# Kernel tuning notes

Measured on AMD Instinct MI355X. Metric: run time of the kernel, lower is better.

Reference implementation:

```python
import jax, jax.numpy as jnp
import numpy as np

N_HEADS = 16
KV_HEADS = 4
HEAD_DIM = 128
D_MODEL = N_HEADS * HEAD_DIM  # 2048
KV_DIM = KV_HEADS * HEAD_DIM  # 512
MAX_POS = 4096
ROPE_THETA = 10000.0
EPS = 1e-5


def _rope_cache(seq_len):
    # QEffMolmoRotaryEmbedding: inv_freq over head_dim, emb = cat(freqs, freqs)
    inv_freq = 1.0 / (ROPE_THETA ** (jnp.arange(0, HEAD_DIM, 2, dtype=jnp.float32) / HEAD_DIM))
    t = jnp.arange(seq_len, dtype=jnp.float32)
    freqs = jnp.outer(t, inv_freq)                      # [S, D/2]
    emb = jnp.concatenate([freqs, freqs], axis=-1)      # [S, D]
    return jnp.cos(emb), jnp.sin(emb)


def _rotate_half(x):
    # x: [B, H, T, D] -> cat(-x2, x1) with halves along last dim
    x1, x2 = jnp.split(x, 2, axis=-1)
    return jnp.concatenate([-x2, x1], axis=-1)


def _rms_norm(x, w):
    var = jnp.mean(jnp.square(x), axis=-1, keepdims=True)
    return (x * jax.lax.rsqrt(var + EPS)) * w


def setup_inputs() -> dict:
    key = jax.random.key(0)
    ks = jax.random.split(key, 8)
    B, T = 1, 2048
    q = jax.random.normal(ks[0], (B, T, D_MODEL), dtype=jnp.float32)
    k = jax.random.normal(ks[1], (B, T, KV_DIM), dtype=jnp.float32)
    v = jax.random.normal(ks[2], (B, T, KV_DIM), dtype=jnp.float32)
    # causal mask: True means masked (torch.where(mask, -10000, scores))
    attention_mask = jnp.triu(jnp.ones((T, T), dtype=bool), k=1)[None, None]  # [1,1,T,T]
    position_ids = jnp.arange(T, dtype=jnp.int32)[None, :]                    # [B,T]
    q_norm_w = jax.random.normal(ks[3], (D_MODEL,), dtype=jnp.float32) * 0.02 + 1.0
    k_norm_w = jax.random.normal(ks[4], (KV_DIM,), dtype=jnp.float32) * 0.02 + 1.0
    w_out = jax.random.normal(ks[5], (D_MODEL, D_MODEL), dtype=jnp.float32) * (D_MODEL ** -0.5)
    return {"q": q, "k": k, "v": v, "attention_mask": attention_mask,
            "position_ids": position_ids, "q_norm_w": q_norm_w,
            "k_norm_w": k_norm_w, "w_out": w_out}


def reference(q, k, v, attention_mask, position_ids, q_norm_w, k_norm_w, w_out):
    B, T, C = q.shape
    # QK-norm on flat projections
    q = _rms_norm(q, q_norm_w)
    k = _rms_norm(k, k_norm_w)
    # split heads: [B, H, T, D]
    q = q.reshape(B, T, N_HEADS, HEAD_DIM).transpose(0, 2, 1, 3)
    k = k.reshape(B, T, KV_HEADS, HEAD_DIM).transpose(0, 2, 1, 3)
    v = v.reshape(B, T, KV_HEADS, HEAD_DIM).transpose(0, 2, 1, 3)
    # RoPE (rotate_half variant)
    cos_c, sin_c = _rope_cache(MAX_POS)
    cos = cos_c[position_ids][:, None]  # [B,1,T,D]
    sin = sin_c[position_ids][:, None]
    q = q * cos + _rotate_half(q) * sin
    k = k * cos + _rotate_half(k) * sin
    # GQA expand
    rep = N_HEADS // KV_HEADS
    k = jnp.repeat(k, rep, axis=1)
    v = jnp.repeat(v, rep, axis=1)
    scale = 1.0 / np.sqrt(HEAD_DIM)
    scores = jnp.einsum('bhqd,bhkd->bhqk', q, k) * scale  # [B,H,T,T]
    scores = jnp.where(attention_mask, jnp.float32(-10000.0), scores)
    attn = jax.nn.softmax(scores.astype(jnp.float32), axis=-1).astype(q.dtype)
    out = jnp.einsum('bhqk,bhkd->bhqd', attn, v)          # [B,H,T,D]
    out = out.transpose(0, 2, 1, 3).reshape(B, T, C)
    return out @ w_out.T
```

## Files before the change

kernel.cpp:

```cpp
#include <hip/hip_runtime.h>
#include <hip/hip_bf16.h>
#include <math.h>

#define T_SEQ 2048
#define NH 16
#define KVH 4
#define HD 128
#define DM 2048
#define KVD 512

typedef short bf16x8 __attribute__((ext_vector_type(8)));
typedef float f32x4 __attribute__((ext_vector_type(4)));
typedef float f32x16 __attribute__((ext_vector_type(16)));
typedef unsigned int uint2v __attribute__((ext_vector_type(2)));

static __device__ __forceinline__ unsigned short f2bf(float f) {
    unsigned int x = __float_as_uint(f);
    x += 0x7fff + ((x >> 16) & 1);
    return (unsigned short)(x >> 16);
}
static __device__ __forceinline__ float bf2f(unsigned short u) {
    return __uint_as_float(((unsigned int)u) << 16);
}

static __device__ __forceinline__ unsigned int cvtpk(float lo, float hi) {
    unsigned int r;
    asm("v_cvt_pk_bf16_f32 %0, %1, %2" : "=v"(r) : "v"(lo), "v"(hi));
    return r;
}

static __device__ __forceinline__ f32x4 mfma16(bf16x8 a, bf16x8 b, f32x4 c) {
    return __builtin_amdgcn_mfma_f32_16x16x32_bf16(a, b, c, 0, 0, 0);
}
static __device__ __forceinline__ f32x16 mfma32(bf16x8 a, bf16x8 b, f32x16 c) {
    return __builtin_amdgcn_mfma_f32_32x32x16_bf16(a, b, c, 0, 0, 0);
}

static __device__ __forceinline__ void gl_lds16(const unsigned short* g, unsigned short* l) {
    __builtin_amdgcn_global_load_lds(
        (const __attribute__((address_space(1))) unsigned int*)g,
        (__attribute__((address_space(3))) unsigned int*)l,
        16, 0, 0);
}


__global__ __launch_bounds__(256) void qk_prep(
    const float* __restrict__ q, const float* __restrict__ k,
    const float* __restrict__ qw, const float* __restrict__ kw,
    const int* __restrict__ pos_ids,
    unsigned short* __restrict__ Qb, unsigned short* __restrict__ Ks) {
    __shared__ float qr[DM];
    __shared__ float kr[KVD];
    __shared__ float cosL[64], sinL[64];
    __shared__ float redq[4], redk[4];
    int t = blockIdx.x, tid = threadIdx.x;

    float qs = 0.f, ks = 0.f;
    {
        const float* qp = q + (size_t)t * DM + tid * 8;
        float4 v0 = *(const float4*)(qp);
        float4 v1 = *(const float4*)(qp + 4);
        float* dst = qr + tid * 8;
        dst[0] = v0.x; dst[1] = v0.y; dst[2] = v0.z; dst[3] = v0.w;
        dst[4] = v1.x; dst[5] = v1.y; dst[6] = v1.z; dst[7] = v1.w;
        qs = v0.x * v0.x + v0.y * v0.y + v0.z * v0.z + v0.w * v0.w +
             v1.x * v1.x + v1.y * v1.y + v1.z * v1.z + v1.w * v1.w;
        float2 kv = *(const float2*)(k + (size_t)t * KVD + tid * 2);
        kr[tid * 2] = kv.x; kr[tid * 2 + 1] = kv.y;
        ks = kv.x * kv.x + kv.y * kv.y;
    }
    if (tid < 64) {
        float pos = (float)pos_ids[t];
        float inv = powf(10000.0f, -(float)tid * (1.0f / 64.0f));
        float a = pos * inv;
        cosL[tid] = cosf(a);
        sinL[tid] = sinf(a);
    }
    for (int off = 32; off; off >>= 1) {
        qs += __shfl_down(qs, off);
        ks += __shfl_down(ks, off);
    }
    if ((tid & 63) == 0) { redq[tid >> 6] = qs; redk[tid >> 6] = ks; }
    __syncthreads();
    float qinv = rsqrtf((redq[0] + redq[1] + redq[2] + redq[3]) * (1.0f / DM) + 1e-5f);
    float kinv = rsqrtf((redk[0] + redk[1] + redk[2] + redk[3]) * (1.0f / KVD) + 1e-5f);

    {
        int base = tid * 8;
        int h = base >> 7;
        int d = base & 127;
        bool lo = d < 64;
        int i0 = d & 63;
        int pb = lo ? base + 64 : base - 64;
        #pragma unroll
        for (int j = 0; j < 8; ++j) {
            float xv = qr[base + j] * qinv * qw[base + j];
            float pv = qr[pb + j] * qinv * qw[pb + j];
            float c = cosL[i0 + j];
            float s = sinL[i0 + j];
            float o = lo ? (xv * c - pv * s) : (xv * c + pv * s);
            Qb[((size_t)h * T_SEQ + t) * HD + d + j] = f2bf(o);
        }
    }
    {
        int base = tid * 2;
        int kh = base >> 7;
        int d = base & 127;
        bool lo = d < 64;
        int i0 = d & 63;
        int pb = lo ? base + 64 : base - 64;
        int kt = t >> 5, lq = t & 31;
        #pragma unroll
        for (int j = 0; j < 2; ++j) {
            float xv = kr[base + j] * kinv * kw[base + j];
            float pv = kr[pb + j] * kinv * kw[pb + j];
            float c = cosL[i0 + j];
            float s = sinL[i0 + j];
            float o = lo ? (xv * c - pv * s) : (xv * c + pv * s);
            int dj = d + j;
            int sl = dj >> 4, hi2 = (dj >> 3) & 1, jj = dj & 7;
            size_t oi = ((((size_t)(kh * 64 + kt) * 8 + sl) * 2 + hi2) * 32 + lq) * 8 + jj;
            Ks[oi] = f2bf(o);
        }
    }
}

__global__ __launch_bounds__(256) void v_prep(const float* __restrict__ v,
                                              unsigned short* __restrict__ Vs) {
    __shared__ unsigned short tile[64][80];
    int tb = blockIdx.x;
    int cb = blockIdx.y;
    int tid = threadIdx.x;
    #pragma unroll 4
    for (int rep = 0; rep < 16; ++rep) {
        int e = rep * 256 + tid;
        int r = e >> 6;
        int c = e & 63;
        tile[c][r] = f2bf(v[(size_t)(tb * 64 + r) * KVD + cb * 64 + c]);
    }
    __syncthreads();
    #pragma unroll
    for (int rep = 0; rep < 2; ++rep) {
        int e = rep * 256 + tid;
        int cc = e >> 3, tg = e & 7;
        int cg = cb * 64 + cc;
        int kh = cg >> 7, crow = cg & 127, db = crow >> 5, lq = crow & 31;
        int t0g = tb * 64 + tg * 8;
        int kt = t0g >> 5, tr = t0g & 31, half = tr >> 4, hi2 = (tr >> 3) & 1;
        size_t o = (((((size_t)(kh * 64 + kt) * 2 + half) * 4 + db) * 2 + hi2) * 32 + lq) * 8;
        *(bf16x8*)(Vs + o) = *(const bf16x8*)(&tile[cc][tg * 8]);
    }
}

__global__ __launch_bounds__(256) void w_prep(const float* __restrict__ w,
                                              unsigned short* __restrict__ Wb) {
    size_t idx = ((size_t)blockIdx.x * 256 + threadIdx.x) * 4;
    float4 f = *(const float4*)(w + idx);
    ushort4 o;
    o.x = f2bf(f.x); o.y = f2bf(f.y); o.z = f2bf(f.z); o.w = f2bf(f.w);
    *(ushort4*)(Wb + idx) = o;
}

#define BEXP 20.0f
#define SCALE2 (0.08838834764831845f * 1.4426950408889634f)

#define STAGE(B, KT)                                                               \
    do {                                                                           \
        const unsigned short* kg_ = Kt_g + (size_t)(KT) * 4096;                    \
        const unsigned short* vg_ = Vt_g + (size_t)(KT) * 4096;                    \
        gl_lds16(kg_ + w * 512 + l * 8,        &kv[B][w * 512]);                   \
        gl_lds16(kg_ + 2048 + w * 512 + l * 8, &kv[B][2048 + w * 512]);            \
        gl_lds16(vg_ + w * 512 + l * 8,        &kv[B][4096 + w * 512]);            \
        gl_lds16(vg_ + 2048 + w * 512 + l * 8, &kv[B][6144 + w * 512]);            \
    } while (0)

__global__ __launch_bounds__(256) void attn_fwd14(
    const unsigned short* __restrict__ Qb, const unsigned short* __restrict__ Ks,
    const unsigned short* __restrict__ Vs,
    unsigned short* __restrict__ Opart, float* __restrict__ Lpart,
    unsigned short* __restrict__ Xo, int CHUNK) {
    int qrow = 63 - (int)blockIdx.x;
    int kh = blockIdx.y;
    int seg = blockIdx.z;
    int tid = threadIdx.x;
    int w = tid >> 6, l = tid & 63;
    int h = kh * 4 + w;
    int lq = l & 31, hi = l >> 5;
    int qglob = qrow * 32 + lq;

    int nkt = qrow + 1;
    int t0 = seg * CHUNK;
    int t1 = min(t0 + CHUNK, nkt);
    if (t0 >= t1) return;
    size_t idx = (size_t)(h * 64 + qrow) * 8 + seg;

    const unsigned short* Qh = Qb + (size_t)h * T_SEQ * HD;
    const unsigned short* Kt_g = Ks + (size_t)kh * 64 * 4096;
    const unsigned short* Vt_g = Vs + (size_t)kh * 64 * 4096;

    __shared__ unsigned short kv[2][8192];

    bf16x8 qf[8];
    #pragma unroll
    for (int sl = 0; sl < 8; ++sl)
        qf[sl] = *(const bf16x8*)(Qh + (size_t)qglob * HD + sl * 16 + hi * 8);

    f32x16 oacc[4];
    #pragma unroll
    for (int db = 0; db < 4; ++db)
        #pragma unroll
        for (int r = 0; r < 16; ++r) oacc[db][r] = 0.f;
    f32x4 sden4 = (f32x4){0.f, 0.f, 0.f, 0.f};

    STAGE(0, t0);
    if (t0 + 1 < t1) STAGE(1, t0 + 1);
    int cur = 0;
    for (int kt = t0; kt < t1; ++kt) {
        if (kt + 1 < t1) asm volatile("s_waitcnt vmcnt(4)" ::: "memory");
        else             asm volatile("s_waitcnt vmcnt(0)" ::: "memory");
        __builtin_amdgcn_s_barrier();
        const unsigned short* kl = &kv[cur][0] + l * 8;
        const unsigned short* vl = &kv[cur][4096] + l * 8;
        f32x16 sa, sb;
        #pragma unroll
        for (int r = 0; r < 16; ++r) { sa[r] = 0.f; sb[r] = 0.f; }
        #pragma unroll
        for (int x = 0; x < 8; x += 2) {
            bf16x8 k0 = *(const bf16x8*)(kl + x * 512);
            bf16x8 k1 = *(const bf16x8*)(kl + (x + 1) * 512);
            sa = mfma32(k0, qf[x], sa);
            sb = mfma32(k1, qf[x + 1], sb);
        }
        float p_[16];
        if (kt == nkt - 1) {
            int lim = qglob - kt * 32;
            #pragma unroll
            for (int r = 0; r < 16; ++r) {
                float e_ = __builtin_amdgcn_exp2f((sa[r] + sb[r]) * SCALE2 - BEXP);
                int off_ = (r & 3) + 8 * (r >> 2) + 4 * hi;
                p_[r] = (off_ <= lim) ? e_ : 0.f;
                sden4[r & 3] += p_[r];
            }
        } else {
            #pragma unroll
            for (int r = 0; r < 16; ++r) {
                p_[r] = __builtin_amdgcn_exp2f((sa[r] + sb[r]) * SCALE2 - BEXP);
                sden4[r & 3] += p_[r];
            }
        }
        #pragma unroll
        for (int half = 0; half < 2; ++half) {
            unsigned int a0 = cvtpk(p_[half * 8 + 0], p_[half * 8 + 1]);
            unsigned int a1 = cvtpk(p_[half * 8 + 2], p_[half * 8 + 3]);
            unsigned int b0 = cvtpk(p_[half * 8 + 4], p_[half * 8 + 5]);
            unsigned int b1 = cvtpk(p_[half * 8 + 6], p_[half * 8 + 7]);
            uint2v w0 = __builtin_amdgcn_permlane32_swap(a0, b0, false, false);
            uint2v w1 = __builtin_amdgcn_permlane32_swap(a1, b1, false, false);
            union { unsigned int u[4]; bf16x8 v; } pc;
            pc.u[0] = w0[0]; pc.u[1] = w1[0]; pc.u[2] = w0[1]; pc.u[3] = w1[1];
            bf16x8 pf = pc.v;
            #pragma unroll
            for (int db = 0; db < 4; ++db) {
                bf16x8 vf = *(const bf16x8*)(vl + (half * 4 + db) * 512);
                oacc[db] = mfma32(vf, pf, oacc[db]);
            }
        }
        asm volatile("s_waitcnt lgkmcnt(0)" ::: "memory");
        __builtin_amdgcn_s_barrier();
        if (kt + 2 < t1) STAGE(cur, kt + 2);
        cur ^= 1;
    }

    float sden = (sden4[0] + sden4[1]) + (sden4[2] + sden4[3]);
    float sden_tot = sden + __shfl_xor(sden, 32);

    if (t0 == 0 && t1 == nkt) {
        float invs = 1.0f / sden_tot;
        #pragma unroll
        for (int db = 0; db < 4; ++db) {
            #pragma unroll
            for (int r = 0; r < 16; ++r) {
                int d = db * 32 + (r & 3) + 8 * (r >> 2) + 4 * hi;
                Xo[(size_t)qglob * DM + h * HD + d] = f2bf(oacc[db][r] * invs);
            }
        }
        return;
    }
    if (hi == 0) Lpart[idx * 32 + lq] = sden_tot;
    unsigned short* op = Opart + (idx << 12);
    #pragma unroll
    for (int db = 0; db < 4; ++db) {
        #pragma unroll
        for (int r = 0; r < 16; ++r) {
            int d = db * 32 + (r & 3) + 8 * (r >> 2) + 4 * hi;
            op[d * 32 + lq] = f2bf(oacc[db][r]);
        }
    }
}

__global__ __launch_bounds__(256) void attn_combine(
    const unsigned short* __restrict__ Opart, const float* __restrict__ Lpart,
    unsigned short* __restrict__ Xo, int CHUNK) {
    int qrow = CHUNK + blockIdx.x;
    int h = blockIdx.y;
    int tid = threadIdx.x;
    int nkt = qrow + 1;
    int used = (nkt + CHUNK - 1) / CHUNK;
    int base = (h * 64 + qrow) * 8;
    __shared__ float invden[32];
    if (tid < 32) {
        int q = tid;
        float den = 0.f;
        for (int s = 0; s < used; ++s) den += Lpart[(base + s) * 32 + q];
        invden[q] = 1.0f / den;
    }
    __syncthreads();
    int d = tid >> 1, q0 = (tid & 1) * 16;
    float acc[16];
    #pragma unroll
    for (int j = 0; j < 16; ++j) acc[j] = 0.f;
    for (int s = 0; s < used; ++s) {
        const unsigned short* op = Opart + ((size_t)(base + s) << 12) + d * 32 + q0;
        bf16x8 o0 = *(const bf16x8*)(op);
        bf16x8 o1 = *(const bf16x8*)(op + 8);
        #pragma unroll
        for (int j = 0; j < 8; ++j) {
            acc[j]     += bf2f((unsigned short)o0[j]);
            acc[8 + j] += bf2f((unsigned short)o1[j]);
        }
    }
    __shared__ unsigned short xo[32][136];
    #pragma unroll
    for (int j = 0; j < 16; ++j)
        xo[q0 + j][d] = f2bf(acc[j] * invden[q0 + j]);
    __syncthreads();
    int q = tid >> 3, dc = (tid & 7) * 16;
    bf16x8 v0 = *(const bf16x8*)(&xo[q][dc]);
    bf16x8 v1 = *(const bf16x8*)(&xo[q][dc + 8]);
    size_t ro = (size_t)(qrow * 32 + q) * DM + h * HD + dc;
    *(bf16x8*)(Xo + ro) = v0;
    *(bf16x8*)(Xo + ro + 8) = v1;
}

__global__ __launch_bounds__(256) void outproj2(
    const unsigned short* __restrict__ X, const unsigned short* __restrict__ Wb,
    float* __restrict__ out) {
    __shared__ unsigned short As[128][72];
    __shared__ unsigned short Bs[64][72];
    int tid = threadIdx.x;
    int w = tid >> 6, l = tid & 63;
    int lr = l & 15, lg = l >> 4;
    int wm = w >> 1, wn = w & 1;
    int id = blockIdx.x;
    int wg = (id & 7) * 64 + (id >> 3);
    int m0 = (wg & 15) * 128, n0 = (wg >> 4) * 64;

    int ar_row[4], ar_col[4], br_row[2], br_col[2];
    #pragma unroll
    for (int qd = 0; qd < 4; ++qd) {
        int c = tid + qd * 256;
        ar_row[qd] = c >> 3; ar_col[qd] = (c & 7) * 8;
    }
    #pragma unroll
    for (int qd = 0; qd < 2; ++qd) {
        int c = tid + qd * 256;
        br_row[qd] = c >> 3; br_col[qd] = (c & 7) * 8;
    }

    f32x4 acc[4][2];
    #pragma unroll
    for (int i = 0; i < 4; ++i)
        #pragma unroll
        for (int j = 0; j < 2; ++j) acc[i][j] = (f32x4){0.f, 0.f, 0.f, 0.f};

    bf16x8 ar[4], br[2];
    #pragma unroll
    for (int qd = 0; qd < 4; ++qd)
        ar[qd] = *(const bf16x8*)(X + (size_t)(m0 + ar_row[qd]) * DM + ar_col[qd]);
    #pragma unroll
    for (int qd = 0; qd < 2; ++qd)
        br[qd] = *(const bf16x8*)(Wb + (size_t)(n0 + br_row[qd]) * DM + br_col[qd]);
    #pragma unroll
    for (int qd = 0; qd < 4; ++qd)
        *(bf16x8*)(&As[ar_row[qd]][ar_col[qd]]) = ar[qd];
    #pragma unroll
    for (int qd = 0; qd < 2; ++qd)
        *(bf16x8*)(&Bs[br_row[qd]][br_col[qd]]) = br[qd];
    __syncthreads();

    for (int t = 0; t < DM / 64; ++t) {
        if (t + 1 < DM / 64) {
            int k0 = (t + 1) * 64;
            #pragma unroll
            for (int qd = 0; qd < 4; ++qd)
                ar[qd] = *(const bf16x8*)(X + (size_t)(m0 + ar_row[qd]) * DM + k0 + ar_col[qd]);
            #pragma unroll
            for (int qd = 0; qd < 2; ++qd)
                br[qd] = *(const bf16x8*)(Wb + (size_t)(n0 + br_row[qd]) * DM + k0 + br_col[qd]);
        }
        #pragma unroll
        for (int ks = 0; ks < 2; ++ks) {
            bf16x8 af[4], bfr[2];
            #pragma unroll
            for (int i = 0; i < 4; ++i)
                af[i] = *(const bf16x8*)(&As[wm * 64 + i * 16 + lr][ks * 32 + lg * 8]);
            #pragma unroll
            for (int j = 0; j < 2; ++j)
                bfr[j] = *(const bf16x8*)(&Bs[wn * 32 + j * 16 + lr][ks * 32 + lg * 8]);
            #pragma unroll
            for (int i = 0; i < 4; ++i)
                #pragma unroll
                for (int j = 0; j < 2; ++j)
                    acc[i][j] = mfma16(af[i], bfr[j], acc[i][j]);
        }
        if (t + 1 < DM / 64) {
            __syncthreads();
            #pragma unroll
            for (int qd = 0; qd < 4; ++qd)
                *(bf16x8*)(&As[ar_row[qd]][ar_col[qd]]) = ar[qd];
            #pragma unroll
            for (int qd = 0; qd < 2; ++qd)
                *(bf16x8*)(&Bs[br_row[qd]][br_col[qd]]) = br[qd];
            __syncthreads();
        }
    }
    #pragma unroll
    for (int i = 0; i < 4; ++i) {
        #pragma unroll
        for (int j = 0; j < 2; ++j) {
            #pragma unroll
            for (int r = 0; r < 4; ++r) {
                int row = m0 + wm * 64 + i * 16 + lg * 4 + r;
                int col = n0 + wn * 32 + j * 16 + lr;
                out[(size_t)row * DM + col] = acc[i][j][r];
            }
        }
    }
}

extern "C" void kernel_launch(void* const* d_in, const int* in_sizes, int n_in,
                              void* d_out, int out_size, void* d_ws, size_t ws_size,
                              hipStream_t stream) {
    const float* q = (const float*)d_in[0];
    const float* k = (const float*)d_in[1];
    const float* v = (const float*)d_in[2];
    const int* pos_ids = (const int*)d_in[4];
    const float* qw = (const float*)d_in[5];
    const float* kw = (const float*)d_in[6];
    const float* wout = (const float*)d_in[7];
    float* out = (float*)d_out;

    char* ws = (char*)d_ws;
    unsigned short* Qb = (unsigned short*)(ws + 0x100000);
    unsigned short* Ks = (unsigned short*)(ws + 0x900000);
    unsigned short* Vs = (unsigned short*)(ws + 0xB00000);
    unsigned short* Wb = (unsigned short*)(ws + 0xD00000);
    unsigned short* Xo = (unsigned short*)(ws + 0x1500000);
    float* Lpart = (float*)(ws + 0x1D00000);
    unsigned short* Opart = (unsigned short*)(ws + 0x1E00000);

    int CHUNK = (ws_size >= 0x1E00000ull + 8ull * 0x800000ull) ? 8 : 64;
    int zsegs = (CHUNK == 8) ? 8 : 1;

    qk_prep<<<T_SEQ, 256, 0, stream>>>(q, k, qw, kw, pos_ids, Qb, Ks);
    v_prep<<<dim3(T_SEQ / 64, KVD / 64), 256, 0, stream>>>(v, Vs);
    w_prep<<<(DM * DM) / (256 * 4), 256, 0, stream>>>(wout, Wb);
    attn_fwd14<<<dim3(64, KVH, zsegs), 256, 0, stream>>>(Qb, Ks, Vs, Opart, Lpart, Xo, CHUNK);
    if (CHUNK == 8)
        attn_combine<<<dim3(64 - 8, NH), 256, 0, stream>>>(Opart, Lpart, Xo, CHUNK);
    outproj2<<<512, 256, 0, stream>>>(Xo, Wb, out);
}
```

Before: 99.53 us.

## Process two query tiles per wave to reuse staged K/V tiles

```diff
diff --git a/kernel.cpp b/kernel.cpp
--- a/kernel.cpp
+++ b/kernel.cpp
@@ -174,25 +174,26 @@
         gl_lds16(vg_ + 2048 + w * 512 + l * 8, &kv[B][6144 + w * 512]);            \
     } while (0)
 
-__global__ __launch_bounds__(256) void attn_fwd14(
+__global__ __launch_bounds__(256, 2) void attn_fwd15(
     const unsigned short* __restrict__ Qb, const unsigned short* __restrict__ Ks,
     const unsigned short* __restrict__ Vs,
     unsigned short* __restrict__ Opart, float* __restrict__ Lpart,
     unsigned short* __restrict__ Xo, int CHUNK) {
-    int qrow = 63 - (int)blockIdx.x;
+    int qpair = 31 - (int)blockIdx.x;
     int kh = blockIdx.y;
     int seg = blockIdx.z;
     int tid = threadIdx.x;
     int w = tid >> 6, l = tid & 63;
     int h = kh * 4 + w;
     int lq = l & 31, hi = l >> 5;
-    int qglob = qrow * 32 + lq;
-
-    int nkt = qrow + 1;
+    int qrowA = qpair * 2, qrowB = qrowA + 1;
+    int qgA = qrowA * 32 + lq;
+    int qgB = qrowB * 32 + lq;
+
+    int nkt = qpair * 2 + 2;
     int t0 = seg * CHUNK;
     int t1 = min(t0 + CHUNK, nkt);
     if (t0 >= t1) return;
-    size_t idx = (size_t)(h * 64 + qrow) * 8 + seg;
 
     const unsigned short* Qh = Qb + (size_t)h * T_SEQ * HD;
     const unsigned short* Kt_g = Ks + (size_t)kh * 64 * 4096;
@@ -200,17 +201,20 @@
 
     __shared__ unsigned short kv[2][8192];
 
-    bf16x8 qf[8];
-    #pragma unroll
-    for (int sl = 0; sl < 8; ++sl)
-        qf[sl] = *(const bf16x8*)(Qh + (size_t)qglob * HD + sl * 16 + hi * 8);
-
-    f32x16 oacc[4];
+    bf16x8 qfA[8], qfB[8];
+    #pragma unroll
+    for (int sl = 0; sl < 8; ++sl) {
+        qfA[sl] = *(const bf16x8*)(Qh + (size_t)qgA * HD + sl * 16 + hi * 8);
+        qfB[sl] = *(const bf16x8*)(Qh + (size_t)qgB * HD + sl * 16 + hi * 8);
+    }
+
+    f32x16 oA[4], oB[4];
     #pragma unroll
     for (int db = 0; db < 4; ++db)
         #pragma unroll
-        for (int r = 0; r < 16; ++r) oacc[db][r] = 0.f;
-    f32x4 sden4 = (f32x4){0.f, 0.f, 0.f, 0.f};
+        for (int r = 0; r < 16; ++r) { oA[db][r] = 0.f; oB[db][r] = 0.f; }
+    f32x4 sdA = (f32x4){0.f, 0.f, 0.f, 0.f};
+    f32x4 sdB = (f32x4){0.f, 0.f, 0.f, 0.f};
 
     STAGE(0, t0);
     if (t0 + 1 < t1) STAGE(1, t0 + 1);
@@ -225,44 +229,59 @@
         #pragma unroll
         for (int r = 0; r < 16; ++r) { sa[r] = 0.f; sb[r] = 0.f; }
         #pragma unroll
-        for (int x = 0; x < 8; x += 2) {
-            bf16x8 k0 = *(const bf16x8*)(kl + x * 512);
-            bf16x8 k1 = *(const bf16x8*)(kl + (x + 1) * 512);
-            sa = mfma32(k0, qf[x], sa);
-            sb = mfma32(k1, qf[x + 1], sb);
-        }
-        float p_[16];
-        if (kt == nkt - 1) {
-            int lim = qglob - kt * 32;
+        for (int x = 0; x < 8; ++x) {
+            bf16x8 kf = *(const bf16x8*)(kl + x * 512);
+            sa = mfma32(kf, qfA[x], sa);
+            sb = mfma32(kf, qfB[x], sb);
+        }
+        float pA[16], pB[16];
+        if (kt >= nkt - 2) {
+            int limA = qgA - kt * 32;
+            int limB = qgB - kt * 32;
             #pragma unroll
             for (int r = 0; r < 16; ++r) {
-                float e_ = __builtin_amdgcn_exp2f((sa[r] + sb[r]) * SCALE2 - BEXP);
                 int off_ = (r & 3) + 8 * (r >> 2) + 4 * hi;
-                p_[r] = (off_ <= lim) ? e_ : 0.f;
-                sden4[r & 3] += p_[r];
+                float eA = __builtin_amdgcn_exp2f(sa[r] * SCALE2 - BEXP);
+                float eB = __builtin_amdgcn_exp2f(sb[r] * SCALE2 - BEXP);
+                pA[r] = (off_ <= limA) ? eA : 0.f;
+                pB[r] = (off_ <= limB) ? eB : 0.f;
+                sdA[r & 3] += pA[r];
+                sdB[r & 3] += pB[r];
             }
         } else {
             #pragma unroll
             for (int r = 0; r < 16; ++r) {
-                p_[r] = __builtin_amdgcn_exp2f((sa[r] + sb[r]) * SCALE2 - BEXP);
-                sden4[r & 3] += p_[r];
+                pA[r] = __builtin_amdgcn_exp2f(sa[r] * SCALE2 - BEXP);
+                pB[r] = __builtin_amdgcn_exp2f(sb[r] * SCALE2 - BEXP);
+                sdA[r & 3] += pA[r];
+                sdB[r & 3] += pB[r];
             }
         }
         #pragma unroll
         for (int half = 0; half < 2; ++half) {
-            unsigned int a0 = cvtpk(p_[half * 8 + 0], p_[half * 8 + 1]);
-            unsigned int a1 = cvtpk(p_[half * 8 + 2], p_[half * 8 + 3]);
-            unsigned int b0 = cvtpk(p_[half * 8 + 4], p_[half * 8 + 5]);
-            unsigned int b1 = cvtpk(p_[half * 8 + 6], p_[half * 8 + 7]);
-            uint2v w0 = __builtin_amdgcn_permlane32_swap(a0, b0, false, false);
-            uint2v w1 = __builtin_amdgcn_permlane32_swap(a1, b1, false, false);
-            union { unsigned int u[4]; bf16x8 v; } pc;
-            pc.u[0] = w0[0]; pc.u[1] = w1[0]; pc.u[2] = w0[1]; pc.u[3] = w1[1];
-            bf16x8 pf = pc.v;
+            unsigned int aA0 = cvtpk(pA[half * 8 + 0], pA[half * 8 + 1]);
+            unsigned int aA1 = cvtpk(pA[half * 8 + 2], pA[half * 8 + 3]);
+            unsigned int bA0 = cvtpk(pA[half * 8 + 4], pA[half * 8 + 5]);
+            unsigned int bA1 = cvtpk(pA[half * 8 + 6], pA[half * 8 + 7]);
+            uint2v wA0 = __builtin_amdgcn_permlane32_swap(aA0, bA0, false, false);
+            uint2v wA1 = __builtin_amdgcn_permlane32_swap(aA1, bA1, false, false);
+            union { unsigned int u[4]; bf16x8 v; } pcA;
+            pcA.u[0] = wA0[0]; pcA.u[1] = wA1[0]; pcA.u[2] = wA0[1]; pcA.u[3] = wA1[1];
+            bf16x8 pfA = pcA.v;
+            unsigned int aB0 = cvtpk(pB[half * 8 + 0], pB[half * 8 + 1]);
+            unsigned int aB1 = cvtpk(pB[half * 8 + 2], pB[half * 8 + 3]);
+            unsigned int bB0 = cvtpk(pB[half * 8 + 4], pB[half * 8 + 5]);
+            unsigned int bB1 = cvtpk(pB[half * 8 + 6], pB[half * 8 + 7]);
+            uint2v wB0 = __builtin_amdgcn_permlane32_swap(aB0, bB0, false, false);
+            uint2v wB1 = __builtin_amdgcn_permlane32_swap(aB1, bB1, false, false);
+            union { unsigned int u[4]; bf16x8 v; } pcB;
+            pcB.u[0] = wB0[0]; pcB.u[1] = wB1[0]; pcB.u[2] = wB0[1]; pcB.u[3] = wB1[1];
+            bf16x8 pfB = pcB.v;
             #pragma unroll
             for (int db = 0; db < 4; ++db) {
                 bf16x8 vf = *(const bf16x8*)(vl + (half * 4 + db) * 512);
-                oacc[db] = mfma32(vf, pf, oacc[db]);
+                oA[db] = mfma32(vf, pfA, oA[db]);
+                oB[db] = mfma32(vf, pfB, oB[db]);
             }
         }
         asm volatile("s_waitcnt lgkmcnt(0)" ::: "memory");
@@ -271,29 +290,39 @@
         cur ^= 1;
     }
 
-    float sden = (sden4[0] + sden4[1]) + (sden4[2] + sden4[3]);
-    float sden_tot = sden + __shfl_xor(sden, 32);
+    float sA = (sdA[0] + sdA[1]) + (sdA[2] + sdA[3]);
+    float sB = (sdB[0] + sdB[1]) + (sdB[2] + sdB[3]);
+    float sAt = sA + __shfl_xor(sA, 32);
+    float sBt = sB + __shfl_xor(sB, 32);
 
     if (t0 == 0 && t1 == nkt) {
-        float invs = 1.0f / sden_tot;
+        float iA = 1.0f / sAt, iB = 1.0f / sBt;
         #pragma unroll
         for (int db = 0; db < 4; ++db) {
             #pragma unroll
             for (int r = 0; r < 16; ++r) {
                 int d = db * 32 + (r & 3) + 8 * (r >> 2) + 4 * hi;
-                Xo[(size_t)qglob * DM + h * HD + d] = f2bf(oacc[db][r] * invs);
+                Xo[(size_t)qgA * DM + h * HD + d] = f2bf(oA[db][r] * iA);
+                Xo[(size_t)qgB * DM + h * HD + d] = f2bf(oB[db][r] * iB);
             }
         }
         return;
     }
-    if (hi == 0) Lpart[idx * 32 + lq] = sden_tot;
-    unsigned short* op = Opart + (idx << 12);
+    size_t idxA = (size_t)(h * 64 + qrowA) * 8 + seg;
+    size_t idxB = (size_t)(h * 64 + qrowB) * 8 + seg;
+    if (hi == 0) {
+        Lpart[idxA * 32 + lq] = sAt;
+        Lpart[idxB * 32 + lq] = sBt;
+    }
+    unsigned short* opA = Opart + (idxA << 12);
+    unsigned short* opB = Opart + (idxB << 12);
     #pragma unroll
     for (int db = 0; db < 4; ++db) {
         #pragma unroll
         for (int r = 0; r < 16; ++r) {
             int d = db * 32 + (r & 3) + 8 * (r >> 2) + 4 * hi;
-            op[d * 32 + lq] = f2bf(oacc[db][r]);
+            opA[d * 32 + lq] = f2bf(oA[db][r]);
+            opB[d * 32 + lq] = f2bf(oB[db][r]);
         }
     }
 }
@@ -304,8 +333,8 @@
     int qrow = CHUNK + blockIdx.x;
     int h = blockIdx.y;
     int tid = threadIdx.x;
-    int nkt = qrow + 1;
-    int used = (nkt + CHUNK - 1) / CHUNK;
+    int nktp = (qrow | 1) + 1;
+    int used = (nktp + CHUNK - 1) / CHUNK;
     int base = (h * 64 + qrow) * 8;
     __shared__ float invden[32];
     if (tid < 32) {
@@ -465,7 +494,7 @@
     qk_prep<<<T_SEQ, 256, 0, stream>>>(q, k, qw, kw, pos_ids, Qb, Ks);
     v_prep<<<dim3(T_SEQ / 64, KVD / 64), 256, 0, stream>>>(v, Vs);
     w_prep<<<(DM * DM) / (256 * 4), 256, 0, stream>>>(wout, Wb);
-    attn_fwd14<<<dim3(64, KVH, zsegs), 256, 0, stream>>>(Qb, Ks, Vs, Opart, Lpart, Xo, CHUNK);
+    attn_fwd15<<<dim3(32, KVH, zsegs), 256, 0, stream>>>(Qb, Ks, Vs, Opart, Lpart, Xo, CHUNK);
     if (CHUNK == 8)
         attn_combine<<<dim3(64 - 8, NH), 256, 0, stream>>>(Opart, Lpart, Xo, CHUNK);
     outproj2<<<512, 256, 0, stream>>>(Xo, Wb, out);
```

New measurement: 138.4 us. +39.0%, slower.
